# Performance work log

Measured on AMD Instinct MI355X. Metric: run time of the kernel, lower is better.

The kernel has to match this reference:

```python
import jax, jax.numpy as jnp
import numpy as np

# Dimensions: B batch, I genes per case, E embed dim, V sga vocab, NH heads,
# NB attention blocks, CAN cancer types, OUT output genes
B, I, E, V, NH, NB, CAN, OUT = 128, 800, 512, 19000, 8, 4, 10, 5000
MASK_VAL = -1e9


def setup_inputs() -> dict:
    key = jax.random.key(0)
    ks = jax.random.split(key, 10)
    s = 0.02
    sga = jax.random.randint(ks[0], (B, I), 0, V)            # 0 == padding
    can = jax.random.randint(ks[1], (B,), 0, CAN)
    emb_tables = jax.random.normal(ks[2], (NB, V + 1, E), jnp.float32) * s
    emb_tables = emb_tables.at[:, 0, :].set(0.0)              # padding_idx=0
    Wk = jax.random.normal(ks[3], (NB, E, E), jnp.float32) * s   # transform2Keys
    bk = jnp.zeros((NB, E), jnp.float32)
    Wq = jax.random.normal(ks[4], (NB, E, NH), jnp.float32) * s  # queryKeyMatch
    bq = jnp.zeros((NB, NH), jnp.float32)
    can_emb = jax.random.normal(ks[5], (CAN, E), jnp.float32) * s
    Wh = jax.random.normal(ks[6], (NB - 1, E, E), jnp.float32) * s  # residual linears (no bias)
    Wfinal = jax.random.normal(ks[7], (E, OUT), jnp.float32) * s    # final linear (no bias)
    return dict(sga=sga, can=can, emb_tables=emb_tables, Wk=Wk, bk=bk,
                Wq=Wq, bq=bq, can_emb=can_emb, Wh=Wh, Wfinal=Wfinal)


def _sga_block(sga, table, Wk_b, bk_b, Wq_b, bq_b):
    embs = table[sga]                                   # [B,I,E] gather
    keys = jnp.tanh(embs @ Wk_b + bk_b)                 # [B,I,E]
    scores = keys @ Wq_b + bq_b                         # [B,I,NH]
    scores = jnp.where(sga[..., None] == 0, MASK_VAL, scores)
    A = jax.nn.softmax(scores, axis=1)                  # softmax over genes I
    emb = jnp.einsum('bin,bie->be', A, embs)            # sum over heads + genes
    attn_wt = A.sum(axis=2)                             # [B,I]
    return emb, attn_wt


def reference(sga, can, emb_tables, Wk, bk, Wq, bq, can_emb, Wh, Wfinal):
    emb0, attn0 = _sga_block(sga, emb_tables[0], Wk[0], bk[0], Wq[0], bq[0])
    curr = jax.nn.relu(emb0 + can_emb[can])             # using_cancer_type=True
    attns = [attn0]
    hiddens = [curr]
    for i in range(1, NB):
        emb_i, attn_i = _sga_block(sga, emb_tables[i], Wk[i], bk[i], Wq[i], bq[i])
        curr = emb_i + curr @ Wh[i - 1]
        curr = jax.nn.relu(curr) if i < NB - 1 else jax.nn.sigmoid(curr)
        attns.append(attn_i)
        hiddens.append(curr)
    preds = curr @ Wfinal                               # [B,OUT]
    return preds, jnp.stack(attns), jnp.stack(hiddens)
```

## Files before the change

### kernel.cpp

```cpp
#include <hip/hip_runtime.h>
#include <hip/hip_bf16.h>

constexpr int Bn   = 128;
constexpr int In   = 800;
constexpr int En   = 512;
constexpr int V1   = 19001;
constexpr int NHn  = 8;
constexpr int NBn  = 4;
constexpr int OUTn = 5000;

constexpr int OFF_ATTN = Bn * OUTn;
constexpr int OFF_HID  = OFF_ATTN + NBn * Bn * In;

typedef __attribute__((ext_vector_type(8))) short bf16x8;
typedef __attribute__((ext_vector_type(8))) unsigned short u16x8;
typedef __attribute__((ext_vector_type(4))) float f32x4;

__device__ inline ushort f2bf(float x) {
    __hip_bfloat16 h = __float2bfloat16(x);
    return *reinterpret_cast<ushort*>(&h);
}
__device__ inline float bf2f(ushort u) {
    return __uint_as_float(((unsigned)u) << 16);
}
__device__ inline void gl_lds16(const ushort* g, ushort* l) {
    __builtin_amdgcn_global_load_lds(
        (const __attribute__((address_space(1))) void*)g,
        (__attribute__((address_space(3))) void*)l, 16, 0, 0);
}

__global__ __launch_bounds__(256)
void k_prep(const float* __restrict__ Wk, ushort* __restrict__ Wkt) {
    __shared__ float ts[64][65];
    const int n0 = blockIdx.x * 64, k0 = blockIdx.y * 64, nb = blockIdx.z;
    const int t = threadIdx.x;
    {
        const int kr = t >> 2, nc = (t & 3) * 16;
        const float* p = Wk + (((size_t)nb * En) + (k0 + kr)) * En + n0 + nc;
#pragma unroll
        for (int j = 0; j < 4; ++j) {
            const float4 v = *(const float4*)(p + j * 4);
            ts[kr][nc + j * 4 + 0] = v.x; ts[kr][nc + j * 4 + 1] = v.y;
            ts[kr][nc + j * 4 + 2] = v.z; ts[kr][nc + j * 4 + 3] = v.w;
        }
    }
    __syncthreads();
    {
        const int nr = t >> 2, kc = (t & 3) * 16;
        ushort* d = Wkt + (((size_t)nb * En) + (n0 + nr)) * En + k0 + kc;
        ushort4 o;
#pragma unroll
        for (int j = 0; j < 4; ++j) {
            o.x = f2bf(ts[kc + j * 4 + 0][nr]); o.y = f2bf(ts[kc + j * 4 + 1][nr]);
            o.z = f2bf(ts[kc + j * 4 + 2][nr]); o.w = f2bf(ts[kc + j * 4 + 3][nr]);
            *(ushort4*)(d + j * 4) = o;
        }
    }
}

template <bool TBF>
__global__ __launch_bounds__(256, 2)
void k_scores(const float* __restrict__ T, const ushort* __restrict__ Wkt,
              const float* __restrict__ bk, const float* __restrict__ Wq,
              float* __restrict__ scoresv, ushort* __restrict__ Tbf) {
    __shared__ ushort Bs[2][512][32];
    __shared__ union { ushort A[2][64][32]; float red[4][64][NHn]; } u;

    const int mblk = blockIdx.x, nb = blockIdx.y;
    const int v0 = mblk * 64;
    const int tid = threadIdx.x, lane = tid & 63, w = tid >> 6;
    const int q = lane >> 4, c = lane & 15;

    const float*  Tb = T + (size_t)nb * V1 * En;
    const ushort* Wn = Wkt + (size_t)nb * En * En;

    const int arow = tid >> 2, akq = tid & 3;
    const int vra = v0 + arow;
    const float* agp = Tb + (size_t)vra * En + akq * 8;
    ushort* tsp = Tbf + ((size_t)nb * V1 + vra) * En + akq * 8;

    f32x4 acc[4][8];
#pragma unroll
    for (int mt = 0; mt < 4; ++mt)
#pragma unroll
        for (int nt = 0; nt < 8; ++nt) acc[mt][nt] = (f32x4)0.0f;

    auto stageB = [&](int buf, int k0) {
#pragma unroll
        for (int j = 0; j < 8; ++j) {
            const int nrow = (w * 8 + j) * 16;
            const ushort* gp =
                Wn + (size_t)(nrow + (lane >> 2)) * En + k0 + (lane & 3) * 8;
            gl_lds16(gp, &Bs[buf][nrow][0]);
        }
    };
    auto loadA = [&](int k0, float4& f0, float4& f1) {
        if (vra < V1) {
            f0 = *(const float4*)(agp + k0);
            f1 = *(const float4*)(agp + k0 + 4);
        } else {
            f0 = make_float4(0.f, 0.f, 0.f, 0.f);
            f1 = f0;
        }
    };
    auto writeA = [&](int buf, int k0, float4 f0, float4 f1) {
        u16x8 o;
        o[0] = f2bf(f0.x); o[1] = f2bf(f0.y); o[2] = f2bf(f0.z); o[3] = f2bf(f0.w);
        o[4] = f2bf(f1.x); o[5] = f2bf(f1.y); o[6] = f2bf(f1.z); o[7] = f2bf(f1.w);
        *(u16x8*)&u.A[buf][arow][akq * 8] = o;
        if (TBF && vra < V1) *(u16x8*)(tsp + k0) = o;
    };

    stageB(0, 0);
    {
        float4 f0, f1;
        loadA(0, f0, f1);
        writeA(0, 0, f0, f1);
    }
    __syncthreads();

    for (int it = 0; it < 16; ++it) {
        const int cur = it & 1, nxt = cur ^ 1;
        const int k0n = (it + 1) * 32;
        float4 p0, p1;
        if (it < 15) {
            stageB(nxt, k0n);
            loadA(k0n, p0, p1);
        }
        bf16x8 aF[4], bF[8];
#pragma unroll
        for (int mt = 0; mt < 4; ++mt)
            aF[mt] = *(bf16x8*)&u.A[cur][mt * 16 + c][q * 8];
#pragma unroll
        for (int nt = 0; nt < 8; ++nt)
            bF[nt] = *(bf16x8*)&Bs[cur][w * 128 + nt * 16 + c][q * 8];
#pragma unroll
        for (int nt = 0; nt < 8; ++nt)
#pragma unroll
            for (int mt = 0; mt < 4; ++mt)
                acc[mt][nt] = __builtin_amdgcn_mfma_f32_16x16x32_bf16(
                    aF[mt], bF[nt], acc[mt][nt], 0, 0, 0);
        if (it < 15) writeA(nxt, k0n, p0, p1);
        __syncthreads();
    }

#pragma unroll
    for (int nt = 0; nt < 8; ++nt) {
        const int col = w * 128 + nt * 16 + c;
        const float bkv = bk[nb * En + col];
#pragma unroll
        for (int mt = 0; mt < 4; ++mt)
#pragma unroll
            for (int r = 0; r < 4; ++r)
                acc[mt][nt][r] = tanhf(acc[mt][nt][r] + bkv);
    }

    for (int h = 0; h < NHn; ++h) {
        float wqh[8];
#pragma unroll
        for (int nt = 0; nt < 8; ++nt) {
            const int col = w * 128 + nt * 16 + c;
            wqh[nt] = Wq[((size_t)nb * En + col) * NHn + h];
        }
        float p[4][4];
#pragma unroll
        for (int mt = 0; mt < 4; ++mt)
#pragma unroll
            for (int r = 0; r < 4; ++r) {
                float s = 0.f;
#pragma unroll
                for (int nt = 0; nt < 8; ++nt) s += acc[mt][nt][r] * wqh[nt];
                p[mt][r] = s;
            }
#pragma unroll
        for (int m = 1; m < 16; m <<= 1) {
#pragma unroll
            for (int mt = 0; mt < 4; ++mt)
#pragma unroll
                for (int r = 0; r < 4; ++r)
                    p[mt][r] += __shfl_xor(p[mt][r], m, 64);
        }
        if (c == h) {
#pragma unroll
            for (int mt = 0; mt < 4; ++mt)
#pragma unroll
                for (int r = 0; r < 4; ++r)
                    u.red[w][mt * 16 + q * 4 + r][h] = p[mt][r];
        }
    }
    __syncthreads();

    for (int idx = tid; idx < 64 * NHn; idx += 256) {
        const int row = idx >> 3, h = idx & 7;
        const int vr = v0 + row;
        if (vr < V1)
            scoresv[((size_t)nb * V1 + vr) * NHn + h] =
                u.red[0][row][h] + u.red[1][row][h] +
                u.red[2][row][h] + u.red[3][row][h];
    }
}

__global__ __launch_bounds__(256)
void k_softmax(const int* __restrict__ sga, const float* __restrict__ scoresv,
               float* __restrict__ attn_out) {
    const int b  = blockIdx.x;
    const int nb = blockIdx.y;
    const int tid = threadIdx.x;
    const int lane = tid & 63;
    const int wid  = tid >> 6;
    __shared__ float red[4 * NHn];

    float sc[4][NHn];
    int ivals[4];
#pragma unroll
    for (int s = 0; s < 4; ++s) {
        const int i = tid + s * 256;
        ivals[s] = i;
        if (i < In) {
            const int v = sga[b * In + i];
            const float4 s0 = *(const float4*)(scoresv + ((size_t)nb * V1 + v) * NHn);
            const float4 s1 = *(const float4*)(scoresv + ((size_t)nb * V1 + v) * NHn + 4);
            sc[s][0] = s0.x; sc[s][1] = s0.y; sc[s][2] = s0.z; sc[s][3] = s0.w;
            sc[s][4] = s1.x; sc[s][5] = s1.y; sc[s][6] = s1.z; sc[s][7] = s1.w;
            if (v == 0) {
#pragma unroll
                for (int n = 0; n < NHn; ++n) sc[s][n] = -1e9f;
            }
        } else {
#pragma unroll
            for (int n = 0; n < NHn; ++n) sc[s][n] = -3.0e38f;
        }
    }

    float lm[NHn];
#pragma unroll
    for (int n = 0; n < NHn; ++n)
        lm[n] = fmaxf(fmaxf(sc[0][n], sc[1][n]), fmaxf(sc[2][n], sc[3][n]));
#pragma unroll
    for (int m = 1; m < 64; m <<= 1) {
#pragma unroll
        for (int n = 0; n < NHn; ++n) lm[n] = fmaxf(lm[n], __shfl_xor(lm[n], m, 64));
    }
    if (lane == 0) {
#pragma unroll
        for (int n = 0; n < NHn; ++n) red[wid * NHn + n] = lm[n];
    }
    __syncthreads();
    float M[NHn];
#pragma unroll
    for (int n = 0; n < NHn; ++n)
        M[n] = fmaxf(fmaxf(red[n], red[NHn + n]), fmaxf(red[2 * NHn + n], red[3 * NHn + n]));
    __syncthreads();

    float ls[NHn];
#pragma unroll
    for (int n = 0; n < NHn; ++n) ls[n] = 0.f;
#pragma unroll
    for (int s = 0; s < 4; ++s) {
#pragma unroll
        for (int n = 0; n < NHn; ++n) {
            sc[s][n] = expf(sc[s][n] - M[n]);
            ls[n] += sc[s][n];
        }
    }
#pragma unroll
    for (int m = 1; m < 64; m <<= 1) {
#pragma unroll
        for (int n = 0; n < NHn; ++n) ls[n] += __shfl_xor(ls[n], m, 64);
    }
    if (lane == 0) {
#pragma unroll
        for (int n = 0; n < NHn; ++n) red[wid * NHn + n] = ls[n];
    }
    __syncthreads();
    float inv[NHn];
#pragma unroll
    for (int n = 0; n < NHn; ++n) {
        const float S = red[n] + red[NHn + n] + red[2 * NHn + n] + red[3 * NHn + n];
        inv[n] = 1.0f / S;
    }

#pragma unroll
    for (int s = 0; s < 4; ++s) {
        if (ivals[s] < In) {
            float w = 0.f;
#pragma unroll
            for (int n = 0; n < NHn; ++n) w += sc[s][n] * inv[n];
            attn_out[((size_t)nb * Bn + b) * In + ivals[s]] = w;
        }
    }
}

template <bool TBF>
__global__ __launch_bounds__(512)
void k_emb(const int* __restrict__ sga, const float* __restrict__ attn,
           const float* __restrict__ T, const ushort* __restrict__ Tbf,
           float* __restrict__ emb) {
    const int b  = blockIdx.x;
    const int nb = blockIdx.y;
    __shared__ int   sv[In];
    __shared__ float sw[In];
    __shared__ float pa[8][En];
    for (int idx = threadIdx.x; idx < In; idx += 512) {
        sv[idx] = sga[b * In + idx];
        sw[idx] = attn[((size_t)nb * Bn + b) * In + idx];
    }
    __syncthreads();
    const int wave = threadIdx.x >> 6, lane = threadIdx.x & 63;
    float a[8];
#pragma unroll
    for (int j = 0; j < 8; ++j) a[j] = 0.f;

    if (TBF) {
        const ushort* Tb = Tbf + (size_t)nb * V1 * En;
#pragma unroll 4
        for (int g = 0; g < 100; ++g) {
            const int i = wave * 100 + g;
            const int v = sv[i];
            const float w = sw[i];
            const u16x8 t = *(const u16x8*)(Tb + (size_t)v * En + lane * 8);
#pragma unroll
            for (int j = 0; j < 8; ++j) a[j] += w * bf2f(t[j]);
        }
    } else {
        const float* Tb = T + (size_t)nb * V1 * En;
#pragma unroll 4
        for (int g = 0; g < 100; ++g) {
            const int i = wave * 100 + g;
            const int v = sv[i];
            const float w = sw[i];
            const float4* p = (const float4*)(Tb + (size_t)v * En) + lane * 2;
            const float4 t0 = p[0], t1 = p[1];
            a[0] += w * t0.x; a[1] += w * t0.y; a[2] += w * t0.z; a[3] += w * t0.w;
            a[4] += w * t1.x; a[5] += w * t1.y; a[6] += w * t1.z; a[7] += w * t1.w;
        }
    }
#pragma unroll
    for (int j = 0; j < 8; ++j) pa[wave][lane * 8 + j] = a[j];
    __syncthreads();
    const int t = threadIdx.x;
    float s = 0.f;
#pragma unroll
    for (int wv = 0; wv < 8; ++wv) s += pa[wv][t];
    emb[((size_t)nb * Bn + b) * En + t] = s;
}

__global__ __launch_bounds__(256)
void k_step0(const float* __restrict__ emb0, const int* __restrict__ can,
             const float* __restrict__ can_emb, float* __restrict__ cur,
             float* __restrict__ hid) {
    const int b = blockIdx.x;
    const int e0 = threadIdx.x * 2;
    const int c = can[b];
    float2 v = *(const float2*)(emb0 + (size_t)b * En + e0);
    const float2 ce = *(const float2*)(can_emb + (size_t)c * En + e0);
    v.x = fmaxf(v.x + ce.x, 0.f);
    v.y = fmaxf(v.y + ce.y, 0.f);
    *(float2*)(cur + (size_t)b * En + e0) = v;
    *(float2*)(hid + (size_t)b * En + e0) = v;
}

__global__ __launch_bounds__(256)
void k_step(const float* __restrict__ embi, const float* __restrict__ prev,
            const float* __restrict__ Whi, float* __restrict__ cur,
            float* __restrict__ hid, const int sig) {
    const int b = blockIdx.x, cc = blockIdx.y;
    __shared__ float pr[En];
    __shared__ float part[2][128];
    pr[threadIdx.x]       = prev[(size_t)b * En + threadIdx.x];
    pr[threadIdx.x + 256] = prev[(size_t)b * En + threadIdx.x + 256];
    __syncthreads();
    const int col = cc * 128 + (threadIdx.x & 127);
    const int kh  = threadIdx.x >> 7;
    float s = 0.f;
    const float* Wp = Whi + (size_t)(kh * 256) * En + col;
#pragma unroll 8
    for (int k = 0; k < 256; ++k) s += pr[kh * 256 + k] * Wp[(size_t)k * En];
    part[kh][threadIdx.x & 127] = s;
    __syncthreads();
    if (threadIdx.x < 128) {
        float a = part[0][threadIdx.x] + part[1][threadIdx.x] +
                  embi[(size_t)b * En + col];
        if (sig) a = 1.0f / (1.0f + expf(-a));
        else     a = fmaxf(a, 0.f);
        cur[(size_t)b * En + col] = a;
        hid[(size_t)b * En + col] = a;
    }
}

__global__ __launch_bounds__(256, 2)
void k_preds(const float* __restrict__ cur, const float* __restrict__ Wf,
             float* __restrict__ preds) {
    __shared__ float cs[32 * En];
    const int nt = blockIdx.x;
    const int bt = blockIdx.y;
    for (int idx = threadIdx.x; idx < 32 * 128; idx += 256) {
        const int row = idx >> 7;
        const int c4  = (idx & 127) << 2;
        *(float4*)(cs + row * En + c4) =
            *(const float4*)(cur + (size_t)(bt * 32 + row) * En + c4);
    }
    __syncthreads();
    const int lane = threadIdx.x & 63;
    const int rgrp = threadIdx.x >> 6;
    const int col = nt * 64 + lane;
    float acc[8];
#pragma unroll
    for (int j = 0; j < 8; ++j) acc[j] = 0.f;
    const bool ok = (col < OUTn);
    for (int k = 0; k < En; k += 4) {
        float w0 = 0.f, w1 = 0.f, w2 = 0.f, w3 = 0.f;
        if (ok) {
            w0 = Wf[(size_t)(k + 0) * OUTn + col];
            w1 = Wf[(size_t)(k + 1) * OUTn + col];
            w2 = Wf[(size_t)(k + 2) * OUTn + col];
            w3 = Wf[(size_t)(k + 3) * OUTn + col];
        }
#pragma unroll
        for (int j = 0; j < 8; ++j) {
            const float4 cv = *(const float4*)(cs + (rgrp * 8 + j) * En + k);
            acc[j] += cv.x * w0 + cv.y * w1 + cv.z * w2 + cv.w * w3;
        }
    }
    if (ok) {
#pragma unroll
        for (int j = 0; j < 8; ++j)
            preds[(size_t)(bt * 32 + rgrp * 8 + j) * OUTn + col] = acc[j];
    }
}

extern "C" void kernel_launch(void* const* d_in, const int* in_sizes, int n_in,
                              void* d_out, int out_size, void* d_ws, size_t ws_size,
                              hipStream_t stream) {
    const int*   sga     = (const int*)d_in[0];
    const int*   can     = (const int*)d_in[1];
    const float* T       = (const float*)d_in[2];
    const float* Wk      = (const float*)d_in[3];
    const float* bk      = (const float*)d_in[4];
    const float* Wq      = (const float*)d_in[5];
    const float* can_emb = (const float*)d_in[7];
    const float* Wh      = (const float*)d_in[8];
    const float* Wf      = (const float*)d_in[9];

    float* out = (float*)d_out;
    float* ws  = (float*)d_ws;

    float* scoresv = ws;
    float* embw    = scoresv + (size_t)NBn * V1 * NHn;
    float* cur0    = embw + (size_t)NBn * Bn * En;
    float* cur1    = cur0 + (size_t)Bn * En;
    ushort* Wkt    = (ushort*)(cur1 + (size_t)Bn * En);
    ushort* Tbf    = Wkt + (size_t)NBn * En * En;
    const size_t need_full =
        (size_t)(scoresv - ws) * 4 +
        ((size_t)NBn * V1 * NHn + (size_t)NBn * Bn * En + 2 * (size_t)Bn * En) * 4 +
        (size_t)NBn * En * En * 2 + (size_t)NBn * V1 * En * 2;
    const bool useTbf = (ws_size >= need_full);

    float* preds_out = out;
    float* attn_out  = out + OFF_ATTN;
    float* hid_out   = out + OFF_HID;

    k_prep<<<dim3(8, 8, NBn), 256, 0, stream>>>(Wk, Wkt);
    if (useTbf)
        k_scores<true><<<dim3((V1 + 63) / 64, NBn), 256, 0, stream>>>(
            T, Wkt, bk, Wq, scoresv, Tbf);
    else
        k_scores<false><<<dim3((V1 + 63) / 64, NBn), 256, 0, stream>>>(
            T, Wkt, bk, Wq, scoresv, Tbf);
    k_softmax<<<dim3(Bn, NBn), 256, 0, stream>>>(sga, scoresv, attn_out);
    if (useTbf)
        k_emb<true><<<dim3(Bn, NBn), 512, 0, stream>>>(sga, attn_out, T, Tbf, embw);
    else
        k_emb<false><<<dim3(Bn, NBn), 512, 0, stream>>>(sga, attn_out, T, Tbf, embw);
    k_step0<<<Bn, 256, 0, stream>>>(embw, can, can_emb, cur0, hid_out);
    k_step<<<dim3(Bn, 4), 256, 0, stream>>>(embw + 1 * Bn * En, cur0,
                                            Wh + 0 * En * En, cur1,
                                            hid_out + 1 * (size_t)Bn * En, 0);
    k_step<<<dim3(Bn, 4), 256, 0, stream>>>(embw + 2 * Bn * En, cur1,
                                            Wh + 1 * En * En, cur0,
                                            hid_out + 2 * (size_t)Bn * En, 0);
    k_step<<<dim3(Bn, 4), 256, 0, stream>>>(embw + 3 * Bn * En, cur0,
                                            Wh + 2 * En * En, cur1,
                                            hid_out + 3 * (size_t)Bn * En, 1);
    k_preds<<<dim3((OUTn + 63) / 64, Bn / 32), 256, 0, stream>>>(cur1, Wf, preds_out);
}
```

Baseline: 576.4 us.

## Bucket gene indices by vocab with histogram/scan and rewrite scores GEMM without LDS

Adds a counting-sort pipeline (histogram, scan, fill) that groups each batch half's gene occurrences by vocab id. A new embedding kernel then walks vocab segments so table rows are read in sorted order, accumulating into shared-memory per-batch accumulators and flushing with atomics. The scores GEMM drops LDS staging and double buffering, reads A and B fragments straight from global memory with 32-row tiles, and raises occupancy to 3 blocks. This adds several small kernel launches, a serial single-block scan, and atomic contention in exchange for better cache locality on the table gather.

```diff
diff --git a/kernel.cpp b/kernel.cpp
--- a/kernel.cpp
+++ b/kernel.cpp
@@ -9,6 +9,9 @@
 constexpr int NBn  = 4;
 constexpr int OUTn = 5000;
 
+constexpr int NVP  = 19008;
+constexpr int NBIN = 2 * NVP;
+
 constexpr int OFF_ATTN = Bn * OUTn;
 constexpr int OFF_HID  = OFF_ATTN + NBn * Bn * In;
 
@@ -23,10 +26,8 @@
 __device__ inline float bf2f(ushort u) {
     return __uint_as_float(((unsigned)u) << 16);
 }
-__device__ inline void gl_lds16(const ushort* g, ushort* l) {
-    __builtin_amdgcn_global_load_lds(
-        (const __attribute__((address_space(1))) void*)g,
-        (__attribute__((address_space(3))) void*)l, 16, 0, 0);
+__device__ inline bf16x8 asbf(u16x8 u) {
+    union { u16x8 u; bf16x8 b; } x; x.u = u; return x.b;
 }
 
 __global__ __launch_bounds__(256)
@@ -58,145 +59,174 @@
     }
 }
 
+__global__ __launch_bounds__(256)
+void k_zero(float* __restrict__ p, int n) {
+    const int i = blockIdx.x * 256 + threadIdx.x;
+    if (i < n) p[i] = 0.f;
+}
+
+__global__ __launch_bounds__(256)
+void k_hist(const int* __restrict__ sga, int* __restrict__ cnt) {
+    const int idx = blockIdx.x * 256 + threadIdx.x;
+    if (idx < Bn * In) {
+        const int v = sga[idx];
+        const int b = idx / In;
+        atomicAdd(&cnt[(b >> 6) * NVP + v], 1);
+    }
+}
+
+__global__ __launch_bounds__(256)
+void k_scan(const int* __restrict__ cnt, int* __restrict__ offs,
+            int* __restrict__ cursor) {
+    __shared__ int tsum[256];
+    const int t = threadIdx.x;
+    const int CH = 149;
+    const int base = t * CH;
+    int s = 0;
+    for (int j = 0; j < CH; ++j) {
+        const int idx = base + j;
+        if (idx < NBIN) s += cnt[idx];
+    }
+    tsum[t] = s;
+    __syncthreads();
+    for (int off = 1; off < 256; off <<= 1) {
+        const int v = (t >= off) ? tsum[t - off] : 0;
+        __syncthreads();
+        tsum[t] += v;
+        __syncthreads();
+    }
+    int running = (t == 0) ? 0 : tsum[t - 1];
+    for (int j = 0; j < CH; ++j) {
+        const int idx = base + j;
+        if (idx < NBIN) {
+            const int cv = cnt[idx];
+            offs[idx] = running;
+            cursor[idx] = running;
+            running += cv;
+        }
+    }
+    if (t == 255) offs[NBIN] = running;
+}
+
+__global__ __launch_bounds__(256)
+void k_fill(const int* __restrict__ sga, int* __restrict__ cursor,
+            int2* __restrict__ payload) {
+    const int idx = blockIdx.x * 256 + threadIdx.x;
+    if (idx < Bn * In) {
+        const int v = sga[idx];
+        const int b = idx / In;
+        const int i = idx - b * In;
+        const int pos = atomicAdd(&cursor[(b >> 6) * NVP + v], 1);
+        payload[pos] = make_int2(v, (b << 10) | i);
+    }
+}
+
 template <bool TBF>
-__global__ __launch_bounds__(256, 2)
+__global__ __launch_bounds__(256, 3)
 void k_scores(const float* __restrict__ T, const ushort* __restrict__ Wkt,
               const float* __restrict__ bk, const float* __restrict__ Wq,
               float* __restrict__ scoresv, ushort* __restrict__ Tbf) {
-    __shared__ ushort Bs[2][512][32];
-    __shared__ union { ushort A[2][64][32]; float red[4][64][NHn]; } u;
-
-    const int mblk = blockIdx.x, nb = blockIdx.y;
-    const int v0 = mblk * 64;
-    const int tid = threadIdx.x, lane = tid & 63, w = tid >> 6;
+    __shared__ float red[4][32][NHn];
+    const int v0 = blockIdx.x * 32, nb = blockIdx.y;
+    const int tid = threadIdx.x, lane = tid & 63, wv = tid >> 6;
     const int q = lane >> 4, c = lane & 15;
 
     const float*  Tb = T + (size_t)nb * V1 * En;
     const ushort* Wn = Wkt + (size_t)nb * En * En;
 
-    const int arow = tid >> 2, akq = tid & 3;
-    const int vra = v0 + arow;
-    const float* agp = Tb + (size_t)vra * En + akq * 8;
-    ushort* tsp = Tbf + ((size_t)nb * V1 + vra) * En + akq * 8;
-
-    f32x4 acc[4][8];
-#pragma unroll
-    for (int mt = 0; mt < 4; ++mt)
+    const int vr0 = v0 + c, vr1 = v0 + 16 + c;
+    const bool ok0 = vr0 < V1, ok1 = vr1 < V1;
+    const float* a0p = Tb + (size_t)vr0 * En + q * 8;
+    const float* a1p = Tb + (size_t)vr1 * En + q * 8;
+    ushort* t0p = Tbf + ((size_t)nb * V1 + vr0) * En + q * 8;
+    ushort* t1p = Tbf + ((size_t)nb * V1 + vr1) * En + q * 8;
+
+    const ushort* bp[8];
+#pragma unroll
+    for (int nt = 0; nt < 8; ++nt)
+        bp[nt] = Wn + (size_t)(wv * 128 + nt * 16 + c) * En + q * 8;
+
+    f32x4 acc[2][8];
+#pragma unroll
+    for (int mt = 0; mt < 2; ++mt)
 #pragma unroll
         for (int nt = 0; nt < 8; ++nt) acc[mt][nt] = (f32x4)0.0f;
 
-    auto stageB = [&](int buf, int k0) {
-#pragma unroll
-        for (int j = 0; j < 8; ++j) {
-            const int nrow = (w * 8 + j) * 16;
-            const ushort* gp =
-                Wn + (size_t)(nrow + (lane >> 2)) * En + k0 + (lane & 3) * 8;
-            gl_lds16(gp, &Bs[buf][nrow][0]);
-        }
-    };
-    auto loadA = [&](int k0, float4& f0, float4& f1) {
-        if (vra < V1) {
-            f0 = *(const float4*)(agp + k0);
-            f1 = *(const float4*)(agp + k0 + 4);
-        } else {
-            f0 = make_float4(0.f, 0.f, 0.f, 0.f);
-            f1 = f0;
-        }
-    };
-    auto writeA = [&](int buf, int k0, float4 f0, float4 f1) {
-        u16x8 o;
-        o[0] = f2bf(f0.x); o[1] = f2bf(f0.y); o[2] = f2bf(f0.z); o[3] = f2bf(f0.w);
-        o[4] = f2bf(f1.x); o[5] = f2bf(f1.y); o[6] = f2bf(f1.z); o[7] = f2bf(f1.w);
-        *(u16x8*)&u.A[buf][arow][akq * 8] = o;
-        if (TBF && vra < V1) *(u16x8*)(tsp + k0) = o;
-    };
-
-    stageB(0, 0);
-    {
-        float4 f0, f1;
-        loadA(0, f0, f1);
-        writeA(0, 0, f0, f1);
-    }
-    __syncthreads();
-
+#pragma unroll 2
     for (int it = 0; it < 16; ++it) {
-        const int cur = it & 1, nxt = cur ^ 1;
-        const int k0n = (it + 1) * 32;
-        float4 p0, p1;
-        if (it < 15) {
-            stageB(nxt, k0n);
-            loadA(k0n, p0, p1);
-        }
-        bf16x8 aF[4], bF[8];
-#pragma unroll
-        for (int mt = 0; mt < 4; ++mt)
-            aF[mt] = *(bf16x8*)&u.A[cur][mt * 16 + c][q * 8];
-#pragma unroll
-        for (int nt = 0; nt < 8; ++nt)
-            bF[nt] = *(bf16x8*)&Bs[cur][w * 128 + nt * 16 + c][q * 8];
-#pragma unroll
-        for (int nt = 0; nt < 8; ++nt)
-#pragma unroll
-            for (int mt = 0; mt < 4; ++mt)
-                acc[mt][nt] = __builtin_amdgcn_mfma_f32_16x16x32_bf16(
-                    aF[mt], bF[nt], acc[mt][nt], 0, 0, 0);
-        if (it < 15) writeA(nxt, k0n, p0, p1);
-        __syncthreads();
+        const int k0 = it * 32;
+        u16x8 u0, u1;
+        {
+            float4 f0 = make_float4(0, 0, 0, 0), f1 = f0, g0 = f0, g1 = f0;
+            if (ok0) { f0 = *(const float4*)(a0p + k0); f1 = *(const float4*)(a0p + k0 + 4); }
+            if (ok1) { g0 = *(const float4*)(a1p + k0); g1 = *(const float4*)(a1p + k0 + 4); }
+            u0[0] = f2bf(f0.x); u0[1] = f2bf(f0.y); u0[2] = f2bf(f0.z); u0[3] = f2bf(f0.w);
+            u0[4] = f2bf(f1.x); u0[5] = f2bf(f1.y); u0[6] = f2bf(f1.z); u0[7] = f2bf(f1.w);
+            u1[0] = f2bf(g0.x); u1[1] = f2bf(g0.y); u1[2] = f2bf(g0.z); u1[3] = f2bf(g0.w);
+            u1[4] = f2bf(g1.x); u1[5] = f2bf(g1.y); u1[6] = f2bf(g1.z); u1[7] = f2bf(g1.w);
+        }
+        if (TBF && wv == 0) {
+            if (ok0) *(u16x8*)(t0p + k0) = u0;
+            if (ok1) *(u16x8*)(t1p + k0) = u1;
+        }
+        const bf16x8 a0 = asbf(u0), a1 = asbf(u1);
+#pragma unroll
+        for (int nt = 0; nt < 8; ++nt) {
+            const bf16x8 bF = *(const bf16x8*)(bp[nt] + k0);
+            acc[0][nt] = __builtin_amdgcn_mfma_f32_16x16x32_bf16(a0, bF, acc[0][nt], 0, 0, 0);
+            acc[1][nt] = __builtin_amdgcn_mfma_f32_16x16x32_bf16(a1, bF, acc[1][nt], 0, 0, 0);
+        }
     }
 
 #pragma unroll
     for (int nt = 0; nt < 8; ++nt) {
-        const int col = w * 128 + nt * 16 + c;
-        const float bkv = bk[nb * En + col];
-#pragma unroll
-        for (int mt = 0; mt < 4; ++mt)
+        const float bb = bk[nb * En + wv * 128 + nt * 16 + c];
+#pragma unroll
+        for (int mt = 0; mt < 2; ++mt)
 #pragma unroll
             for (int r = 0; r < 4; ++r)
-                acc[mt][nt][r] = tanhf(acc[mt][nt][r] + bkv);
+                acc[mt][nt][r] = tanhf(acc[mt][nt][r] + bb);
     }
 
     for (int h = 0; h < NHn; ++h) {
         float wqh[8];
 #pragma unroll
-        for (int nt = 0; nt < 8; ++nt) {
-            const int col = w * 128 + nt * 16 + c;
-            wqh[nt] = Wq[((size_t)nb * En + col) * NHn + h];
-        }
-        float p[4][4];
-#pragma unroll
-        for (int mt = 0; mt < 4; ++mt)
+        for (int nt = 0; nt < 8; ++nt)
+            wqh[nt] = Wq[((size_t)nb * En + wv * 128 + nt * 16 + c) * NHn + h];
+        float p0[4], p1[4];
+#pragma unroll
+        for (int r = 0; r < 4; ++r) {
+            float s0 = 0.f, s1 = 0.f;
+#pragma unroll
+            for (int nt = 0; nt < 8; ++nt) {
+                s0 += acc[0][nt][r] * wqh[nt];
+                s1 += acc[1][nt][r] * wqh[nt];
+            }
+            p0[r] = s0; p1[r] = s1;
+        }
+#pragma unroll
+        for (int m = 1; m < 16; m <<= 1) {
 #pragma unroll
             for (int r = 0; r < 4; ++r) {
-                float s = 0.f;
-#pragma unroll
-                for (int nt = 0; nt < 8; ++nt) s += acc[mt][nt][r] * wqh[nt];
-                p[mt][r] = s;
+                p0[r] += __shfl_xor(p0[r], m, 64);
+                p1[r] += __shfl_xor(p1[r], m, 64);
             }
-#pragma unroll
-        for (int m = 1; m < 16; m <<= 1) {
-#pragma unroll
-            for (int mt = 0; mt < 4; ++mt)
-#pragma unroll
-                for (int r = 0; r < 4; ++r)
-                    p[mt][r] += __shfl_xor(p[mt][r], m, 64);
         }
         if (c == h) {
 #pragma unroll
-            for (int mt = 0; mt < 4; ++mt)
-#pragma unroll
-                for (int r = 0; r < 4; ++r)
-                    u.red[w][mt * 16 + q * 4 + r][h] = p[mt][r];
-        }
-    }
-    __syncthreads();
-
-    for (int idx = tid; idx < 64 * NHn; idx += 256) {
-        const int row = idx >> 3, h = idx & 7;
+            for (int r = 0; r < 4; ++r) {
+                red[wv][q * 4 + r][h]      = p0[r];
+                red[wv][16 + q * 4 + r][h] = p1[r];
+            }
+        }
+    }
+    __syncthreads();
+    if (tid < 32 * NHn) {
+        const int row = tid >> 3, h = tid & 7;
         const int vr = v0 + row;
         if (vr < V1)
             scoresv[((size_t)nb * V1 + vr) * NHn + h] =
-                u.red[0][row][h] + u.red[1][row][h] +
-                u.red[2][row][h] + u.red[3][row][h];
+                red[0][row][h] + red[1][row][h] + red[2][row][h] + red[3][row][h];
     }
 }
 
@@ -291,11 +321,52 @@
     }
 }
 
-template <bool TBF>
+__global__ __launch_bounds__(256)
+void k_emb2(const int2* __restrict__ payload, const int* __restrict__ offs,
+            const float* __restrict__ attn, const ushort* __restrict__ Tbf,
+            float* __restrict__ embw) {
+    __shared__ float acc[64][256];
+    const int seg = blockIdx.x;
+    const int eh  = blockIdx.y & 1;
+    const int bh  = blockIdx.y >> 1;
+    const int nb  = blockIdx.z;
+    const int tid = threadIdx.x, lane = tid & 63, wv = tid >> 6;
+
+    float* af = &acc[0][0];
+    for (int i = tid; i < 64 * 256; i += 256) af[i] = 0.f;
+    __syncthreads();
+
+    const int binlo = bh * NVP + seg * 594;
+    const int e0 = offs[binlo], e1 = offs[binlo + 594];
+    const ushort* Tb = Tbf + (size_t)nb * V1 * En + eh * 256;
+    const float* at = attn + (size_t)nb * Bn * In;
+
+    for (int e = e0; e < e1; ++e) {
+        const int2 pv = payload[e];
+        const int b = pv.y >> 10;
+        if ((b & 3) != wv) continue;
+        const int i = pv.y & 1023;
+        const float w = at[b * In + i];
+        const ushort4 tv = *(const ushort4*)(Tb + (size_t)pv.x * En + lane * 4);
+        float4* ap = (float4*)&acc[b & 63][lane * 4];
+        float4 a = *ap;
+        a.x += w * bf2f(tv.x);
+        a.y += w * bf2f(tv.y);
+        a.z += w * bf2f(tv.z);
+        a.w += w * bf2f(tv.w);
+        *ap = a;
+    }
+    __syncthreads();
+
+    float* dst = embw + ((size_t)nb * Bn + bh * 64) * En + eh * 256 + tid;
+#pragma unroll 4
+    for (int bl = 0; bl < 64; ++bl)
+        atomicAdd(dst + (size_t)bl * En, acc[bl][tid]);
+}
+
 __global__ __launch_bounds__(512)
-void k_emb(const int* __restrict__ sga, const float* __restrict__ attn,
-           const float* __restrict__ T, const ushort* __restrict__ Tbf,
-           float* __restrict__ emb) {
+void k_embf(const int* __restrict__ sga, const float* __restrict__ attn,
+            const float* __restrict__ T, float* __restrict__ emb) {
     const int b  = blockIdx.x;
     const int nb = blockIdx.y;
     __shared__ int   sv[In];
@@ -310,30 +381,16 @@
     float a[8];
 #pragma unroll
     for (int j = 0; j < 8; ++j) a[j] = 0.f;
-
-    if (TBF) {
-        const ushort* Tb = Tbf + (size_t)nb * V1 * En;
+    const float* Tb = T + (size_t)nb * V1 * En;
 #pragma unroll 4
-        for (int g = 0; g < 100; ++g) {
-            const int i = wave * 100 + g;
-            const int v = sv[i];
-            const float w = sw[i];
-            const u16x8 t = *(const u16x8*)(Tb + (size_t)v * En + lane * 8);
-#pragma unroll
-            for (int j = 0; j < 8; ++j) a[j] += w * bf2f(t[j]);
-        }
-    } else {
-        const float* Tb = T + (size_t)nb * V1 * En;
-#pragma unroll 4
-        for (int g = 0; g < 100; ++g) {
-            const int i = wave * 100 + g;
-            const int v = sv[i];
-            const float w = sw[i];
-            const float4* p = (const float4*)(Tb + (size_t)v * En) + lane * 2;
-            const float4 t0 = p[0], t1 = p[1];
-            a[0] += w * t0.x; a[1] += w * t0.y; a[2] += w * t0.z; a[3] += w * t0.w;
-            a[4] += w * t1.x; a[5] += w * t1.y; a[6] += w * t1.z; a[7] += w * t1.w;
-        }
+    for (int g = 0; g < 100; ++g) {
+        const int i = wave * 100 + g;
+        const int v = sv[i];
+        const float w = sw[i];
+        const float4* p = (const float4*)(Tb + (size_t)v * En) + lane * 2;
+        const float4 t0 = p[0], t1 = p[1];
+        a[0] += w * t0.x; a[1] += w * t0.y; a[2] += w * t0.z; a[3] += w * t0.w;
+        a[4] += w * t1.x; a[5] += w * t1.y; a[6] += w * t1.z; a[7] += w * t1.w;
     }
 #pragma unroll
     for (int j = 0; j < 8; ++j) pa[wave][lane * 8 + j] = a[j];
@@ -445,34 +502,44 @@
     float* out = (float*)d_out;
     float* ws  = (float*)d_ws;
 
-    float* scoresv = ws;
-    float* embw    = scoresv + (size_t)NBn * V1 * NHn;
-    float* cur0    = embw + (size_t)NBn * Bn * En;
-    float* cur1    = cur0 + (size_t)Bn * En;
-    ushort* Wkt    = (ushort*)(cur1 + (size_t)Bn * En);
-    ushort* Tbf    = Wkt + (size_t)NBn * En * En;
-    const size_t need_full =
-        (size_t)(scoresv - ws) * 4 +
-        ((size_t)NBn * V1 * NHn + (size_t)NBn * Bn * En + 2 * (size_t)Bn * En) * 4 +
-        (size_t)NBn * En * En * 2 + (size_t)NBn * V1 * En * 2;
-    const bool useTbf = (ws_size >= need_full);
+    size_t o = 0;
+    auto alloc = [&](size_t n) { size_t r = o; o += (n + 3) & ~(size_t)3; return r; };
+    float* scoresv = ws + alloc(608032);
+    float* embw    = ws + alloc((size_t)NBn * Bn * En);
+    int*   cnt     = (int*)(ws + alloc(NBIN));
+    int*   offs    = (int*)(ws + alloc(NBIN + 1));
+    int*   cursor  = (int*)(ws + alloc(NBIN));
+    int2*  payload = (int2*)(ws + alloc(2 * (size_t)Bn * In));
+    float* cur0    = ws + alloc((size_t)Bn * En);
+    float* cur1    = ws + alloc((size_t)Bn * En);
+    ushort* Wkt    = (ushort*)(ws + alloc((size_t)NBn * En * En / 2));
+    ushort* Tbf    = (ushort*)(ws + alloc((size_t)NBn * V1 * En / 2));
+    const bool useTbf = (ws_size >= o * 4);
 
     float* preds_out = out;
     float* attn_out  = out + OFF_ATTN;
     float* hid_out   = out + OFF_HID;
 
     k_prep<<<dim3(8, 8, NBn), 256, 0, stream>>>(Wk, Wkt);
-    if (useTbf)
-        k_scores<true><<<dim3((V1 + 63) / 64, NBn), 256, 0, stream>>>(
+
+    if (useTbf) {
+        const int nz = NBn * Bn * En + NBIN;
+        k_zero<<<(nz + 255) / 256, 256, 0, stream>>>(embw, nz);
+        k_hist<<<(Bn * In + 255) / 256, 256, 0, stream>>>(sga, cnt);
+        k_scan<<<1, 256, 0, stream>>>(cnt, offs, cursor);
+        k_fill<<<(Bn * In + 255) / 256, 256, 0, stream>>>(sga, cursor, payload);
+        k_scores<true><<<dim3((V1 + 31) / 32, NBn), 256, 0, stream>>>(
             T, Wkt, bk, Wq, scoresv, Tbf);
-    else
-        k_scores<false><<<dim3((V1 + 63) / 64, NBn), 256, 0, stream>>>(
+        k_softmax<<<dim3(Bn, NBn), 256, 0, stream>>>(sga, scoresv, attn_out);
+        k_emb2<<<dim3(32, 4, NBn), 256, 0, stream>>>(payload, offs, attn_out,
+                                                     Tbf, embw);
+    } else {
+        k_scores<false><<<dim3((V1 + 31) / 32, NBn), 256, 0, stream>>>(
             T, Wkt, bk, Wq, scoresv, Tbf);
-    k_softmax<<<dim3(Bn, NBn), 256, 0, stream>>>(sga, scoresv, attn_out);
-    if (useTbf)
-        k_emb<true><<<dim3(Bn, NBn), 512, 0, stream>>>(sga, attn_out, T, Tbf, embw);
-    else
-        k_emb<false><<<dim3(Bn, NBn), 512, 0, stream>>>(sga, attn_out, T, Tbf, embw);
+        k_softmax<<<dim3(Bn, NBn), 256, 0, stream>>>(sga, scoresv, attn_out);
+        k_embf<<<dim3(Bn, NBn), 512, 0, stream>>>(sga, attn_out, T, embw);
+    }
+
     k_step0<<<Bn, 256, 0, stream>>>(embw, can, can_emb, cur0, hid_out);
     k_step<<<dim3(Bn, 4), 256, 0, stream>>>(embw + 1 * Bn * En, cur0,
                                             Wh + 0 * En * En, cur1,
```

Measured after the change: 1.036 ms. 79.7% more time.

## Replace gathered embedding sum with scatter-to-dense weights and split-K MFMA GEMM

Applied to the files above, without the earlier changes.

The attention-weighted embedding sum is reformulated. Attention weights are scattered with atomics into a dense per-batch vocabulary matrix, and that matrix is multiplied by a transposed bf16 copy of the table using split-K MFMA tiles, followed by a reduction kernel. The aim is to replace the irregular per-batch row gathers with a regular tensor-core GEMM. In exchange, the table gets an extra full read and transpose, large buffers must be zeroed, and the attention weights are rounded to bf16. The scores kernel is also retiled to 128x128 blocks without double buffering and no longer writes a bf16 table copy.

```diff
diff --git a/kernel.cpp b/kernel.cpp
--- a/kernel.cpp
+++ b/kernel.cpp
@@ -9,6 +9,10 @@
 constexpr int NBn  = 4;
 constexpr int OUTn = 5000;
 
+constexpr int MPAD = 19072;
+constexpr int KPAD = 19456;
+constexpr int KSn  = 16;
+
 constexpr int OFF_ATTN = Bn * OUTn;
 constexpr int OFF_HID  = OFF_ATTN + NBn * Bn * In;
 
@@ -19,9 +23,6 @@
 __device__ inline ushort f2bf(float x) {
     __hip_bfloat16 h = __float2bfloat16(x);
     return *reinterpret_cast<ushort*>(&h);
-}
-__device__ inline float bf2f(ushort u) {
-    return __uint_as_float(((unsigned)u) << 16);
 }
 __device__ inline void gl_lds16(const ushort* g, ushort* l) {
     __builtin_amdgcn_global_load_lds(
@@ -58,110 +59,135 @@
     }
 }
 
-template <bool TBF>
-__global__ __launch_bounds__(256, 2)
+__global__ __launch_bounds__(256)
+void k_cvt(const float* __restrict__ T, ushort* __restrict__ TbfT) {
+    __shared__ float ts[64][65];
+    const int v0 = blockIdx.x * 64, e0 = blockIdx.y * 64, nb = blockIdx.z;
+    const int t = threadIdx.x;
+    {
+        const int vr = t >> 2, ec = (t & 3) * 16;
+        const int v = v0 + vr;
+        float4 f[4];
+        if (v < V1) {
+            const float* p = T + (((size_t)nb * V1) + v) * En + e0 + ec;
+#pragma unroll
+            for (int j = 0; j < 4; ++j) f[j] = *(const float4*)(p + j * 4);
+        } else {
+#pragma unroll
+            for (int j = 0; j < 4; ++j) f[j] = make_float4(0.f, 0.f, 0.f, 0.f);
+        }
+#pragma unroll
+        for (int j = 0; j < 4; ++j) {
+            ts[vr][ec + j * 4 + 0] = f[j].x; ts[vr][ec + j * 4 + 1] = f[j].y;
+            ts[vr][ec + j * 4 + 2] = f[j].z; ts[vr][ec + j * 4 + 3] = f[j].w;
+        }
+    }
+    __syncthreads();
+    {
+        const int er = t >> 2, vc = (t & 3) * 16;
+        ushort* d = TbfT + (((size_t)nb * En) + (e0 + er)) * KPAD + v0 + vc;
+        ushort4 o;
+#pragma unroll
+        for (int j = 0; j < 4; ++j) {
+            o.x = f2bf(ts[vc + j * 4 + 0][er]); o.y = f2bf(ts[vc + j * 4 + 1][er]);
+            o.z = f2bf(ts[vc + j * 4 + 2][er]); o.w = f2bf(ts[vc + j * 4 + 3][er]);
+            *(ushort4*)(d + j * 4) = o;
+        }
+    }
+}
+
+__global__ __launch_bounds__(256)
+void k_zero(float* __restrict__ p, int n) {
+    const int i = blockIdx.x * 256 + threadIdx.x;
+    if (i < n) p[i] = 0.f;
+}
+
+__global__ __launch_bounds__(256, 3)
 void k_scores(const float* __restrict__ T, const ushort* __restrict__ Wkt,
               const float* __restrict__ bk, const float* __restrict__ Wq,
-              float* __restrict__ scoresv, ushort* __restrict__ Tbf) {
-    __shared__ ushort Bs[2][512][32];
-    __shared__ union { ushort A[2][64][32]; float red[4][64][NHn]; } u;
-
-    const int mblk = blockIdx.x, nb = blockIdx.y;
-    const int v0 = mblk * 64;
-    const int tid = threadIdx.x, lane = tid & 63, w = tid >> 6;
+              float* __restrict__ scoresv) {
+    __shared__ union {
+        struct { ushort A[128][32]; ushort B[128][32]; } s;
+        float red[2][128][NHn];
+    } u;
+    const int mblk = blockIdx.x, nblk = blockIdx.y, nb = blockIdx.z;
+    const int v0 = mblk * 128;
+    const int tid = threadIdx.x, lane = tid & 63, wv = tid >> 6;
+    const int wm = wv & 1, wn = wv >> 1;
     const int q = lane >> 4, c = lane & 15;
 
     const float*  Tb = T + (size_t)nb * V1 * En;
     const ushort* Wn = Wkt + (size_t)nb * En * En;
 
-    const int arow = tid >> 2, akq = tid & 3;
+    const int arow = tid >> 1, ah = tid & 1;
     const int vra = v0 + arow;
-    const float* agp = Tb + (size_t)vra * En + akq * 8;
-    ushort* tsp = Tbf + ((size_t)nb * V1 + vra) * En + akq * 8;
-
-    f32x4 acc[4][8];
+    const float* agp = Tb + (size_t)vra * En + ah * 16;
+    const bool aok = vra < V1;
+
+    f32x4 acc[4][4];
 #pragma unroll
     for (int mt = 0; mt < 4; ++mt)
 #pragma unroll
-        for (int nt = 0; nt < 8; ++nt) acc[mt][nt] = (f32x4)0.0f;
-
-    auto stageB = [&](int buf, int k0) {
-#pragma unroll
-        for (int j = 0; j < 8; ++j) {
-            const int nrow = (w * 8 + j) * 16;
-            const ushort* gp =
-                Wn + (size_t)(nrow + (lane >> 2)) * En + k0 + (lane & 3) * 8;
-            gl_lds16(gp, &Bs[buf][nrow][0]);
-        }
-    };
-    auto loadA = [&](int k0, float4& f0, float4& f1) {
-        if (vra < V1) {
-            f0 = *(const float4*)(agp + k0);
-            f1 = *(const float4*)(agp + k0 + 4);
-        } else {
-            f0 = make_float4(0.f, 0.f, 0.f, 0.f);
-            f1 = f0;
-        }
-    };
-    auto writeA = [&](int buf, int k0, float4 f0, float4 f1) {
-        u16x8 o;
-        o[0] = f2bf(f0.x); o[1] = f2bf(f0.y); o[2] = f2bf(f0.z); o[3] = f2bf(f0.w);
-        o[4] = f2bf(f1.x); o[5] = f2bf(f1.y); o[6] = f2bf(f1.z); o[7] = f2bf(f1.w);
-        *(u16x8*)&u.A[buf][arow][akq * 8] = o;
-        if (TBF && vra < V1) *(u16x8*)(tsp + k0) = o;
-    };
-
-    stageB(0, 0);
-    {
-        float4 f0, f1;
-        loadA(0, f0, f1);
-        writeA(0, 0, f0, f1);
-    }
-    __syncthreads();
+        for (int nt = 0; nt < 4; ++nt) acc[mt][nt] = (f32x4)0.0f;
 
     for (int it = 0; it < 16; ++it) {
-        const int cur = it & 1, nxt = cur ^ 1;
-        const int k0n = (it + 1) * 32;
-        float4 p0, p1;
-        if (it < 15) {
-            stageB(nxt, k0n);
-            loadA(k0n, p0, p1);
-        }
-        bf16x8 aF[4], bF[8];
+        const int k0 = it * 32;
+#pragma unroll
+        for (int j = 0; j < 2; ++j) {
+            const int nr = (wv * 2 + j) * 16;
+            const ushort* gp = Wn + (size_t)(nblk * 128 + nr + (lane >> 2)) * En +
+                               k0 + (lane & 3) * 8;
+            gl_lds16(gp, &u.s.B[nr][0]);
+        }
+        {
+            float4 f0 = make_float4(0, 0, 0, 0), f1 = f0, f2 = f0, f3 = f0;
+            if (aok) {
+                f0 = *(const float4*)(agp + k0);
+                f1 = *(const float4*)(agp + k0 + 4);
+                f2 = *(const float4*)(agp + k0 + 8);
+                f3 = *(const float4*)(agp + k0 + 12);
+            }
+            u16x8 o0, o1;
+            o0[0] = f2bf(f0.x); o0[1] = f2bf(f0.y); o0[2] = f2bf(f0.z); o0[3] = f2bf(f0.w);
+            o0[4] = f2bf(f1.x); o0[5] = f2bf(f1.y); o0[6] = f2bf(f1.z); o0[7] = f2bf(f1.w);
+            o1[0] = f2bf(f2.x); o1[1] = f2bf(f2.y); o1[2] = f2bf(f2.z); o1[3] = f2bf(f2.w);
+            o1[4] = f2bf(f3.x); o1[5] = f2bf(f3.y); o1[6] = f2bf(f3.z); o1[7] = f2bf(f3.w);
+            *(u16x8*)&u.s.A[arow][ah * 16]     = o0;
+            *(u16x8*)&u.s.A[arow][ah * 16 + 8] = o1;
+        }
+        __syncthreads();
+        bf16x8 aF[4], bF[4];
 #pragma unroll
         for (int mt = 0; mt < 4; ++mt)
-            aF[mt] = *(bf16x8*)&u.A[cur][mt * 16 + c][q * 8];
-#pragma unroll
-        for (int nt = 0; nt < 8; ++nt)
-            bF[nt] = *(bf16x8*)&Bs[cur][w * 128 + nt * 16 + c][q * 8];
-#pragma unroll
-        for (int nt = 0; nt < 8; ++nt)
+            aF[mt] = *(bf16x8*)&u.s.A[wm * 64 + mt * 16 + c][q * 8];
+#pragma unroll
+        for (int nt = 0; nt < 4; ++nt)
+            bF[nt] = *(bf16x8*)&u.s.B[wn * 64 + nt * 16 + c][q * 8];
+#pragma unroll
+        for (int nt = 0; nt < 4; ++nt)
 #pragma unroll
             for (int mt = 0; mt < 4; ++mt)
                 acc[mt][nt] = __builtin_amdgcn_mfma_f32_16x16x32_bf16(
                     aF[mt], bF[nt], acc[mt][nt], 0, 0, 0);
-        if (it < 15) writeA(nxt, k0n, p0, p1);
         __syncthreads();
     }
 
 #pragma unroll
-    for (int nt = 0; nt < 8; ++nt) {
-        const int col = w * 128 + nt * 16 + c;
-        const float bkv = bk[nb * En + col];
+    for (int nt = 0; nt < 4; ++nt) {
+        const float bb = bk[nb * En + nblk * 128 + wn * 64 + nt * 16 + c];
 #pragma unroll
         for (int mt = 0; mt < 4; ++mt)
 #pragma unroll
             for (int r = 0; r < 4; ++r)
-                acc[mt][nt][r] = tanhf(acc[mt][nt][r] + bkv);
+                acc[mt][nt][r] = tanhf(acc[mt][nt][r] + bb);
     }
 
     for (int h = 0; h < NHn; ++h) {
-        float wqh[8];
-#pragma unroll
-        for (int nt = 0; nt < 8; ++nt) {
-            const int col = w * 128 + nt * 16 + c;
-            wqh[nt] = Wq[((size_t)nb * En + col) * NHn + h];
-        }
+        float wqh[4];
+#pragma unroll
+        for (int nt = 0; nt < 4; ++nt)
+            wqh[nt] =
+                Wq[((size_t)nb * En + nblk * 128 + wn * 64 + nt * 16 + c) * NHn + h];
         float p[4][4];
 #pragma unroll
         for (int mt = 0; mt < 4; ++mt)
@@ -169,7 +195,7 @@
             for (int r = 0; r < 4; ++r) {
                 float s = 0.f;
 #pragma unroll
-                for (int nt = 0; nt < 8; ++nt) s += acc[mt][nt][r] * wqh[nt];
+                for (int nt = 0; nt < 4; ++nt) s += acc[mt][nt][r] * wqh[nt];
                 p[mt][r] = s;
             }
 #pragma unroll
@@ -177,26 +203,23 @@
 #pragma unroll
             for (int mt = 0; mt < 4; ++mt)
 #pragma unroll
+                for (int r = 0; r < 4; ++r) p[mt][r] += __shfl_xor(p[mt][r], m, 64);
+        }
+        if (c == h) {
+#pragma unroll
+            for (int mt = 0; mt < 4; ++mt)
+#pragma unroll
                 for (int r = 0; r < 4; ++r)
-                    p[mt][r] += __shfl_xor(p[mt][r], m, 64);
-        }
-        if (c == h) {
-#pragma unroll
-            for (int mt = 0; mt < 4; ++mt)
-#pragma unroll
-                for (int r = 0; r < 4; ++r)
-                    u.red[w][mt * 16 + q * 4 + r][h] = p[mt][r];
-        }
-    }
-    __syncthreads();
-
-    for (int idx = tid; idx < 64 * NHn; idx += 256) {
+                    u.red[wn][wm * 64 + mt * 16 + q * 4 + r][h] = p[mt][r];
+        }
+    }
+    __syncthreads();
+    for (int idx = tid; idx < 128 * NHn; idx += 256) {
         const int row = idx >> 3, h = idx & 7;
         const int vr = v0 + row;
         if (vr < V1)
             scoresv[((size_t)nb * V1 + vr) * NHn + h] =
-                u.red[0][row][h] + u.red[1][row][h] +
-                u.red[2][row][h] + u.red[3][row][h];
+                u.red[0][row][h] + u.red[1][row][h];
     }
 }
 
@@ -291,11 +314,108 @@
     }
 }
 
-template <bool TBF>
+__global__ __launch_bounds__(256)
+void k_wfill(const int* __restrict__ sga, const float* __restrict__ attn,
+             float* __restrict__ Wd) {
+    const int idx = blockIdx.x * 256 + threadIdx.x;
+    if (idx >= Bn * In) return;
+    const int b = idx / In, i = idx - b * In;
+    const int v = sga[idx];
+#pragma unroll
+    for (int nb = 0; nb < NBn; ++nb)
+        atomicAdd(Wd + ((size_t)nb * Bn + b) * KPAD + v,
+                  attn[((size_t)nb * Bn + b) * In + i]);
+}
+
+__global__ __launch_bounds__(256, 3)
+void k_emb_gemm(const float* __restrict__ Wd, const ushort* __restrict__ TbfT,
+                float* __restrict__ partial) {
+    __shared__ struct { ushort A[128][32]; ushort B[128][32]; } s;
+    const int eblk = blockIdx.x, ks = blockIdx.y, nb = blockIdx.z;
+    const int tid = threadIdx.x, lane = tid & 63, wv = tid >> 6;
+    const int wm = wv & 1, wn = wv >> 1;
+    const int q = lane >> 4, c = lane & 15;
+
+    const float*  Wb = Wd + (size_t)nb * Bn * KPAD;
+    const ushort* Tt = TbfT + (size_t)nb * En * KPAD;
+
+    const int arow = tid >> 1, ah = tid & 1;
+    const float* agp = Wb + (size_t)arow * KPAD + ah * 16;
+
+    f32x4 acc[4][4];
+#pragma unroll
+    for (int mt = 0; mt < 4; ++mt)
+#pragma unroll
+        for (int nt = 0; nt < 4; ++nt) acc[mt][nt] = (f32x4)0.0f;
+
+    const int kbase = ks * 1216;
+    for (int it = 0; it < 38; ++it) {
+        const int k0 = kbase + it * 32;
+#pragma unroll
+        for (int j = 0; j < 2; ++j) {
+            const int nr = (wv * 2 + j) * 16;
+            const ushort* gp = Tt + (size_t)(eblk * 128 + nr + (lane >> 2)) * KPAD +
+                               k0 + (lane & 3) * 8;
+            gl_lds16(gp, &s.B[nr][0]);
+        }
+        {
+            const float4 f0 = *(const float4*)(agp + k0);
+            const float4 f1 = *(const float4*)(agp + k0 + 4);
+            const float4 f2 = *(const float4*)(agp + k0 + 8);
+            const float4 f3 = *(const float4*)(agp + k0 + 12);
+            u16x8 o0, o1;
+            o0[0] = f2bf(f0.x); o0[1] = f2bf(f0.y); o0[2] = f2bf(f0.z); o0[3] = f2bf(f0.w);
+            o0[4] = f2bf(f1.x); o0[5] = f2bf(f1.y); o0[6] = f2bf(f1.z); o0[7] = f2bf(f1.w);
+            o1[0] = f2bf(f2.x); o1[1] = f2bf(f2.y); o1[2] = f2bf(f2.z); o1[3] = f2bf(f2.w);
+            o1[4] = f2bf(f3.x); o1[5] = f2bf(f3.y); o1[6] = f2bf(f3.z); o1[7] = f2bf(f3.w);
+            *(u16x8*)&s.A[arow][ah * 16]     = o0;
+            *(u16x8*)&s.A[arow][ah * 16 + 8] = o1;
+        }
+        __syncthreads();
+        bf16x8 aF[4], bF[4];
+#pragma unroll
+        for (int mt = 0; mt < 4; ++mt)
+            aF[mt] = *(bf16x8*)&s.A[wm * 64 + mt * 16 + c][q * 8];
+#pragma unroll
+        for (int nt = 0; nt < 4; ++nt)
+            bF[nt] = *(bf16x8*)&s.B[wn * 64 + nt * 16 + c][q * 8];
+#pragma unroll
+        for (int nt = 0; nt < 4; ++nt)
+#pragma unroll
+            for (int mt = 0; mt < 4; ++mt)
+                acc[mt][nt] = __builtin_amdgcn_mfma_f32_16x16x32_bf16(
+                    aF[mt], bF[nt], acc[mt][nt], 0, 0, 0);
+        __syncthreads();
+    }
+
+    float* dst = partial + ((size_t)ks * NBn + nb) * (Bn * En);
+#pragma unroll
+    for (int mt = 0; mt < 4; ++mt)
+#pragma unroll
+        for (int nt = 0; nt < 4; ++nt) {
+            const int e = eblk * 128 + wn * 64 + nt * 16 + c;
+#pragma unroll
+            for (int r = 0; r < 4; ++r) {
+                const int b = wm * 64 + mt * 16 + q * 4 + r;
+                dst[(size_t)b * En + e] = acc[mt][nt][r];
+            }
+        }
+}
+
+__global__ __launch_bounds__(256)
+void k_emb_red(const float* __restrict__ partial, float* __restrict__ embw) {
+    const int i = blockIdx.x * 256 + threadIdx.x;
+    if (i >= NBn * Bn * En) return;
+    float s = 0.f;
+#pragma unroll
+    for (int ks = 0; ks < KSn; ++ks)
+        s += partial[(size_t)ks * (NBn * Bn * En) + i];
+    embw[i] = s;
+}
+
 __global__ __launch_bounds__(512)
-void k_emb(const int* __restrict__ sga, const float* __restrict__ attn,
-           const float* __restrict__ T, const ushort* __restrict__ Tbf,
-           float* __restrict__ emb) {
+void k_embf(const int* __restrict__ sga, const float* __restrict__ attn,
+            const float* __restrict__ T, float* __restrict__ emb) {
     const int b  = blockIdx.x;
     const int nb = blockIdx.y;
     __shared__ int   sv[In];
@@ -310,30 +430,16 @@
     float a[8];
 #pragma unroll
     for (int j = 0; j < 8; ++j) a[j] = 0.f;
-
-    if (TBF) {
-        const ushort* Tb = Tbf + (size_t)nb * V1 * En;
+    const float* Tb = T + (size_t)nb * V1 * En;
 #pragma unroll 4
-        for (int g = 0; g < 100; ++g) {
-            const int i = wave * 100 + g;
-            const int v = sv[i];
-            const float w = sw[i];
-            const u16x8 t = *(const u16x8*)(Tb + (size_t)v * En + lane * 8);
-#pragma unroll
-            for (int j = 0; j < 8; ++j) a[j] += w * bf2f(t[j]);
-        }
-    } else {
-        const float* Tb = T + (size_t)nb * V1 * En;
-#pragma unroll 4
-        for (int g = 0; g < 100; ++g) {
-            const int i = wave * 100 + g;
-            const int v = sv[i];
-            const float w = sw[i];
-            const float4* p = (const float4*)(Tb + (size_t)v * En) + lane * 2;
-            const float4 t0 = p[0], t1 = p[1];
-            a[0] += w * t0.x; a[1] += w * t0.y; a[2] += w * t0.z; a[3] += w * t0.w;
-            a[4] += w * t1.x; a[5] += w * t1.y; a[6] += w * t1.z; a[7] += w * t1.w;
-        }
+    for (int g = 0; g < 100; ++g) {
+        const int i = wave * 100 + g;
+        const int v = sv[i];
+        const float w = sw[i];
+        const float4* p = (const float4*)(Tb + (size_t)v * En) + lane * 2;
+        const float4 t0 = p[0], t1 = p[1];
+        a[0] += w * t0.x; a[1] += w * t0.y; a[2] += w * t0.z; a[3] += w * t0.w;
+        a[4] += w * t1.x; a[5] += w * t1.y; a[6] += w * t1.z; a[7] += w * t1.w;
     }
 #pragma unroll
     for (int j = 0; j < 8; ++j) pa[wave][lane * 8 + j] = a[j];
@@ -445,34 +551,40 @@
     float* out = (float*)d_out;
     float* ws  = (float*)d_ws;
 
-    float* scoresv = ws;
-    float* embw    = scoresv + (size_t)NBn * V1 * NHn;
-    float* cur0    = embw + (size_t)NBn * Bn * En;
-    float* cur1    = cur0 + (size_t)Bn * En;
-    ushort* Wkt    = (ushort*)(cur1 + (size_t)Bn * En);
-    ushort* Tbf    = Wkt + (size_t)NBn * En * En;
-    const size_t need_full =
-        (size_t)(scoresv - ws) * 4 +
-        ((size_t)NBn * V1 * NHn + (size_t)NBn * Bn * En + 2 * (size_t)Bn * En) * 4 +
-        (size_t)NBn * En * En * 2 + (size_t)NBn * V1 * En * 2;
-    const bool useTbf = (ws_size >= need_full);
+    size_t o = 0;
+    auto alloc = [&](size_t n) { size_t r = o; o += (n + 3) & ~(size_t)3; return r; };
+    float* scoresv = ws + alloc((size_t)NBn * V1 * NHn);
+    float* embw    = ws + alloc((size_t)NBn * Bn * En);
+    float* cur0    = ws + alloc((size_t)Bn * En);
+    float* cur1    = ws + alloc((size_t)Bn * En);
+    ushort* Wkt    = (ushort*)(ws + alloc((size_t)NBn * En * En / 2));
+    const size_t small_need = o * 4;
+    float* Wd      = ws + alloc((size_t)NBn * Bn * KPAD);
+    float* partial = ws + alloc((size_t)KSn * NBn * Bn * En);
+    ushort* TbfT   = (ushort*)(ws + alloc((size_t)NBn * En * KPAD / 2));
+    const bool fast = (ws_size >= o * 4);
+    (void)small_need;
 
     float* preds_out = out;
     float* attn_out  = out + OFF_ATTN;
     float* hid_out   = out + OFF_HID;
 
     k_prep<<<dim3(8, 8, NBn), 256, 0, stream>>>(Wk, Wkt);
-    if (useTbf)
-        k_scores<true><<<dim3((V1 + 63) / 64, NBn), 256, 0, stream>>>(
-            T, Wkt, bk, Wq, scoresv, Tbf);
-    else
-        k_scores<false><<<dim3((V1 + 63) / 64, NBn), 256, 0, stream>>>(
-            T, Wkt, bk, Wq, scoresv, Tbf);
+    k_scores<<<dim3(MPAD / 128, 4, NBn), 256, 0, stream>>>(T, Wkt, bk, Wq, scoresv);
     k_softmax<<<dim3(Bn, NBn), 256, 0, stream>>>(sga, scoresv, attn_out);
-    if (useTbf)
-        k_emb<true><<<dim3(Bn, NBn), 512, 0, stream>>>(sga, attn_out, T, Tbf, embw);
-    else
-        k_emb<false><<<dim3(Bn, NBn), 512, 0, stream>>>(sga, attn_out, T, Tbf, embw);
+
+    if (fast) {
+        k_cvt<<<dim3(MPAD / 64, En / 64, NBn), 256, 0, stream>>>(T, TbfT);
+        const int nwd = NBn * Bn * KPAD;
+        k_zero<<<(nwd + 255) / 256, 256, 0, stream>>>(Wd, nwd);
+        k_wfill<<<(Bn * In + 255) / 256, 256, 0, stream>>>(sga, attn_out, Wd);
+        k_emb_gemm<<<dim3(En / 128, KSn, NBn), 256, 0, stream>>>(Wd, TbfT, partial);
+        const int ne = NBn * Bn * En;
+        k_emb_red<<<(ne + 255) / 256, 256, 0, stream>>>(partial, embw);
+    } else {
+        k_embf<<<dim3(Bn, NBn), 512, 0, stream>>>(sga, attn_out, T, embw);
+    }
+
     k_step0<<<Bn, 256, 0, stream>>>(embw, can, can_emb, cur0, hid_out);
     k_step<<<dim3(Bn, 4), 256, 0, stream>>>(embw + 1 * Bn * En, cur0,
                                             Wh + 0 * En * En, cur1,
```

New measurement: 702.9 us. 21.9% more time.
